# Kernel tuning notes

Measured on AMD Instinct MI355X. Metric: run time of the kernel, lower is better.

The kernel has to match this reference:

```python
import jax, jax.numpy as jnp
import numpy as np
import math

EPS = 1e-6          # eps for safe cumprod / clamping
CHUNK = 4           # chunk_size w
SHARP = 1.0         # sharpening_factor
NOISE_STD = 1.0
N_HEADS = 4
ADIM = 512


def moving_sum(x, back, forward):
    """Windowed running sum over last axis: out[k] = sum_{j=k-back}^{k+forward} x[j].
    Equivalent to the conv1d trick in the original (all-ones filter)."""
    k = x.shape[-1]
    pad = [(0, 0)] * (x.ndim - 1) + [(back, forward)]
    c = jnp.cumsum(jnp.pad(x, pad), axis=-1)
    c0 = jnp.concatenate([jnp.zeros_like(c[..., :1]), c], axis=-1)
    w = back + forward
    return c0[..., w + 1: w + 1 + k] - c0[..., :k]


def setup_inputs() -> dict:
    rng = jax.random.key(0)
    ks = jax.random.split(rng, 12)
    B, qlen, klen, kdim, qdim, adim = 8, 256, 2048, 512, 512, ADIM
    s = 0.02
    return {
        "key_enc": jax.random.normal(ks[0], (B, klen, kdim), jnp.float32),
        "query":   jax.random.normal(ks[1], (B, qlen, qdim), jnp.float32),
        "noise":   jax.random.normal(ks[2], (B, qlen, klen), jnp.float32),
        # monotonic energy params
        "Wk_m": jax.random.normal(ks[3], (kdim, adim), jnp.float32) * s,
        "bk_m": jnp.zeros((adim,), jnp.float32),
        "Wq_m": jax.random.normal(ks[4], (qdim, adim), jnp.float32) * s,
        "bq_m": jnp.zeros((adim,), jnp.float32),
        "r":    jnp.array([-4.0], jnp.float32),
        # chunkwise energy params (multi-head)
        "Wk_c": jax.random.normal(ks[5], (kdim, adim), jnp.float32) * s,
        "bk_c": jnp.zeros((adim,), jnp.float32),
        "Wq_c": jax.random.normal(ks[6], (qdim, adim), jnp.float32) * s,
        "bq_c": jnp.zeros((adim,), jnp.float32),
    }


def _mocha_beta(key_enc, query, noise, Wk_m, bk_m, Wq_m, bq_m, r,
                Wk_c, bk_c, Wq_c, bq_c):
    B, klen, _ = key_enc.shape
    qlen = query.shape[1]
    H = N_HEADS
    dk = ADIM // H
    scale = math.sqrt(ADIM)

    # --- monotonic energy (single head): [B, qlen, klen]
    k_m = key_enc @ Wk_m + bk_m
    q_m = query @ Wq_m + bq_m
    e_mono = jnp.einsum('bqa,bka->bqk', q_m, k_m) / scale + r[0]

    # --- p_choose with additive gaussian noise (encourages discreteness)
    p_choose = jax.nn.sigmoid(e_mono + noise * NOISE_STD)  # [B,q,k]

    # --- safe cumprod of (1 - p) via exclusive cumsum in log space
    log1mp = jnp.log(jnp.clip(1.0 - p_choose, EPS, 1.0))
    cumprod_1mp = jnp.exp(jnp.cumsum(log1mp, axis=-1) - log1mp)  # exclusive

    # --- monotonic alpha recurrence over query steps (parallel-mode MoChA)
    aw0 = jnp.zeros((B, klen), jnp.float32).at[:, 0].set(1.0)

    def step(aw_prev, inp):
        p_i, cp_i = inp  # [B, klen]
        alpha_i = p_i * cp_i * jnp.cumsum(
            aw_prev / jnp.clip(cp_i, EPS, 1.0), axis=-1)
        return alpha_i, alpha_i

    xs = (jnp.swapaxes(p_choose, 0, 1), jnp.swapaxes(cumprod_1mp, 0, 1))
    _, alpha_q = jax.lax.scan(step, aw0, xs)          # [q, B, k]
    alpha = jnp.swapaxes(alpha_q, 0, 1)                # [B, q, k]

    # --- chunkwise energy (multi-head): [B, H, q, k]
    k_c = (key_enc @ Wk_c + bk_c).reshape(B, klen, H, dk)
    q_c = (query @ Wq_c + bq_c).reshape(B, qlen, H, dk)
    e_chunk = jnp.einsum('bqhd,bkhd->bhqk', q_c, k_c) / scale

    # --- efficient chunkwise attention (clipped-logit moving-sum softmax)
    e = e_chunk - jnp.max(e_chunk, axis=3, keepdims=True)
    softmax_exp = jnp.maximum(jnp.exp(e), 1e-5)
    denom = moving_sum(softmax_exp, back=CHUNK - 1, forward=0)
    beta = softmax_exp * moving_sum(
        alpha[:, None] * SHARP / denom, back=0, forward=CHUNK - 1)
    return beta  # [B, H, q, k]


def reference(key_enc, query, noise, Wk_m, bk_m, Wq_m, bq_m, r,
              Wk_c, bk_c, Wq_c, bq_c):
    return _mocha_beta(key_enc, query, noise, Wk_m, bk_m, Wq_m, bq_m, r,
                       Wk_c, bk_c, Wq_c, bq_c)
```

## Files before the change

### kernel.cpp

```cpp
#include <hip/hip_runtime.h>
#include <math.h>

#define BATCH   8
#define QLEN    256
#define KLEN    2048
#define KDIM    512
#define NHEADS  4
#define DKH     128
#define NG      5
#define QROWS   (BATCH * QLEN)
#define GCOLS   (NG * 512)

static constexpr float INV_SCALE = 0.04419417382415922f;
static constexpr float EPSV = 1e-6f;

typedef __attribute__((ext_vector_type(8))) short bf16x8;
typedef __attribute__((ext_vector_type(4))) float f32x4;

__device__ __forceinline__ unsigned short f2bf(float f) {
    unsigned u = __builtin_bit_cast(unsigned, f);
    u += 0x7fffu + ((u >> 16) & 1u);
    return (unsigned short)(u >> 16);
}
__device__ __forceinline__ float bf2f(unsigned short u) {
    unsigned x = (unsigned)u << 16;
    return __builtin_bit_cast(float, x);
}

__device__ __forceinline__ void lds_barrier() {
    __asm__ volatile("s_waitcnt lgkmcnt(0)\n\ts_barrier" ::: "memory");
}

__device__ __forceinline__ void gload_lds16(const void* g, void* l) {
    __builtin_amdgcn_global_load_lds(
        (const __attribute__((address_space(1))) void*)g,
        (__attribute__((address_space(3))) void*)l, 16, 0, 0);
}

#define NKXB 8192
#define NQXB 1024
__global__ __launch_bounds__(256) void prep(
    const float* __restrict__ key_enc, const float* __restrict__ query,
    const float* __restrict__ Wk_m, const float* __restrict__ Wk_c,
    const float* __restrict__ Wq_m, const float* __restrict__ Wq_c,
    unsigned short* __restrict__ kx, unsigned short* __restrict__ qx,
    unsigned short* __restrict__ kwm, unsigned short* __restrict__ kwc,
    unsigned short* __restrict__ qwm, unsigned short* __restrict__ qwc)
{
    const int gb = blockIdx.x, tid = threadIdx.x;
    const float* x; unsigned short* y; int i;
    if (gb < NKXB)              { x = key_enc; y = kx; i = gb * 256 + tid; }
    else if (gb < NKXB + NQXB)  { x = query;   y = qx; i = (gb - NKXB) * 256 + tid; }
    else {
        const int w = gb - NKXB - NQXB;
        const int which = w >> 8;
        i = (w & 255) * 256 + tid;
        x = (which == 0) ? Wk_m : (which == 1) ? Wk_c : (which == 2) ? Wq_m : Wq_c;
        y = (which == 0) ? kwm  : (which == 1) ? kwc  : (which == 2) ? qwm  : qwc;
    }
    float4 v = ((const float4*)x)[i];
    ushort4 o;
    o.x = f2bf(v.x); o.y = f2bf(v.y); o.z = f2bf(v.z); o.w = f2bf(v.w);
    ((ushort4*)y)[i] = o;
}

__device__ __forceinline__ void mfma_nt_staged(
    const unsigned short* __restrict__ A, const unsigned short* __restrict__ B,
    int lda, int ldb, int bm, int bn,
    unsigned short* AsLDS, unsigned short* BsLDS, f32x4 acc[4][4], int ksteps)
{
    const int t = threadIdx.x;
    const int wv = t >> 6, ln = t & 63;
    const int r = ln & 15, quad = ln >> 4;
    const int wm = (wv >> 1) * 64, wn = (wv & 1) * 64;
    const int srow = wv * 16 + (ln >> 2);
    const int scol = (ln & 3) * 8;

    for (int ks = 0; ks < ksteps; ++ks) {
        const int k0 = ks * 32;
        #pragma unroll
        for (int j = 0; j < 2; ++j) {
            gload_lds16(A + (size_t)(bm + j * 64 + srow) * lda + k0 + scol,
                        AsLDS + (size_t)(j * 64 + wv * 16) * 32);
            gload_lds16(B + (size_t)(bn + j * 64 + srow) * ldb + k0 + scol,
                        BsLDS + (size_t)(j * 64 + wv * 16) * 32);
        }
        __syncthreads();
        bf16x8 af[4], bg[4];
        #pragma unroll
        for (int f = 0; f < 4; ++f)
            af[f] = *(const bf16x8*)(AsLDS + (size_t)(wm + f * 16 + r) * 32 + quad * 8);
        #pragma unroll
        for (int f = 0; f < 4; ++f)
            bg[f] = *(const bf16x8*)(BsLDS + (size_t)(wn + f * 16 + r) * 32 + quad * 8);
        #pragma unroll
        for (int i = 0; i < 4; ++i)
            #pragma unroll
            for (int j2 = 0; j2 < 4; ++j2)
                acc[i][j2] = __builtin_amdgcn_mfma_f32_16x16x32_bf16(
                    af[i], bg[j2], acc[i][j2], 0, 0, 0);
        __syncthreads();
    }
}

__device__ __forceinline__ void zero_acc(f32x4 acc[4][4]) {
    #pragma unroll
    for (int i = 0; i < 4; ++i)
        #pragma unroll
        for (int j = 0; j < 4; ++j)
            acc[i][j] = f32x4{0.f, 0.f, 0.f, 0.f};
}

__global__ __launch_bounds__(256) void smallg(
    const unsigned short* __restrict__ kwm, const unsigned short* __restrict__ kwc,
    const unsigned short* __restrict__ qwm, const unsigned short* __restrict__ qwc,
    const float* __restrict__ Wk_mf, const float* __restrict__ Wk_cf,
    const float* __restrict__ Wq_mf,
    const float* __restrict__ bq_m, const float* __restrict__ bk_m,
    const float* __restrict__ bq_c,
    unsigned short* __restrict__ GT, float* __restrict__ aux)
{
    __shared__ unsigned short As[128 * 32];
    __shared__ unsigned short Bs[128 * 32];
    __shared__ float red[256];
    const int blk = blockIdx.x, tid = threadIdx.x;

    if (blk < 80) {
        const int seg = blk >> 4, t = blk & 15;
        const int bm = (t >> 2) * 128, bn = (t & 3) * 128;
        const unsigned short *A, *B; int ks;
        if (seg == 0) { A = kwm; B = qwm; ks = 16; }
        else { const int h = seg - 1; A = kwc + h * 128; B = qwc + h * 128; ks = 4; }
        f32x4 acc[4][4]; zero_acc(acc);
        mfma_nt_staged(A, B, 512, 512, bm, bn, As, Bs, acc, ks);
        const int wv = tid >> 6, ln = tid & 63;
        const int r = ln & 15, quad = ln >> 4;
        const int m0 = bm + (wv >> 1) * 64, n0 = bn + (wv & 1) * 64;
        #pragma unroll
        for (int j = 0; j < 4; ++j) {
            const int n = n0 + j * 16 + r;
            #pragma unroll
            for (int i = 0; i < 4; ++i)
                #pragma unroll
                for (int reg = 0; reg < 4; ++reg) {
                    const int m = m0 + i * 16 + quad * 4 + reg;
                    GT[(size_t)(seg * 512 + m) * 512 + n] = f2bf(acc[i][j][reg]);
                }
        }
        return;
    }
    const int ab = blk - 80;
    if (ab < 2) {
        const int d = ab * 256 + tid;
        const float* row = Wk_mf + (size_t)d * 512;
        float s = 0.f;
        for (int j = 0; j < 512; j += 4) {
            float4 a = *(const float4*)(row + j);
            float4 b = *(const float4*)(bq_m + j);
            s += a.x * b.x + a.y * b.y + a.z * b.z + a.w * b.w;
        }
        aux[d] = s; return;
    }
    if (ab < 10) {
        const int t = ab - 2, h = t >> 1;
        const int d = (t & 1) * 256 + tid;
        const float* row = Wk_cf + (size_t)d * 512 + h * 128;
        const float* bv = bq_c + h * 128;
        float s = 0.f;
        for (int j = 0; j < 128; j += 4) {
            float4 a = *(const float4*)(row + j);
            float4 b = *(const float4*)(bv + j);
            s += a.x * b.x + a.y * b.y + a.z * b.z + a.w * b.w;
        }
        aux[512 + h * 512 + d] = s; return;
    }
    if (ab < 12) {
        const int d = (ab - 10) * 256 + tid;
        const float* row = Wq_mf + (size_t)d * 512;
        float s = 0.f;
        for (int j = 0; j < 512; j += 4) {
            float4 a = *(const float4*)(row + j);
            float4 b = *(const float4*)(bk_m + j);
            s += a.x * b.x + a.y * b.y + a.z * b.z + a.w * b.w;
        }
        aux[GCOLS + d] = s; return;
    }
    float s = bq_m[tid] * bk_m[tid] + bq_m[tid + 256] * bk_m[tid + 256];
    red[tid] = s; __syncthreads();
    for (int o = 128; o > 0; o >>= 1) {
        if (tid < o) red[tid] += red[tid + o];
        __syncthreads();
    }
    if (tid == 0) aux[GCOLS + 512] = red[0];
}

__global__ __launch_bounds__(256) void qg_kernel(
    const unsigned short* __restrict__ qx, const unsigned short* __restrict__ GT,
    const float* __restrict__ aux,
    unsigned short* __restrict__ qg, float* __restrict__ vq2)
{
    __shared__ unsigned short As[128 * 32];
    __shared__ unsigned short Bs[128 * 32];
    __shared__ float wuS[512];
    const int v = blockIdx.x, tid = threadIdx.x;
    if (v < 320) {
        const int by = v / 20, bx = v % 20;
        const int bm = by * 128, bn = bx * 128;
        f32x4 acc[4][4]; zero_acc(acc);
        mfma_nt_staged(qx, GT, 512, 512, bm, bn, As, Bs, acc, 16);
        const int wv = tid >> 6, ln = tid & 63;
        const int r = ln & 15, quad = ln >> 4;
        const int m0 = bm + (wv >> 1) * 64, n0 = bn + (wv & 1) * 64;
        #pragma unroll
        for (int j = 0; j < 4; ++j) {
            const int n = n0 + j * 16 + r;
            const float wvb = aux[n];
            #pragma unroll
            for (int i = 0; i < 4; ++i)
                #pragma unroll
                for (int reg = 0; reg < 4; ++reg) {
                    const int m = m0 + i * 16 + quad * 4 + reg;
                    qg[(size_t)m * GCOLS + n] = f2bf(acc[i][j][reg] + wvb);
                }
        }
        return;
    }
    wuS[tid] = aux[GCOLS + tid];
    wuS[tid + 256] = aux[GCOLS + tid + 256];
    __syncthreads();
    const float cc = aux[GCOLS + 512];
    const int q = (v - 320) * 256 + tid;
    const unsigned short* row = qx + (size_t)q * 512;
    float s = 0.f;
    for (int j = 0; j < 512; j += 4) {
        ushort4 a = *(const ushort4*)(row + j);
        s = fmaf(bf2f(a.x), wuS[j], s);
        s = fmaf(bf2f(a.y), wuS[j + 1], s);
        s = fmaf(bf2f(a.z), wuS[j + 2], s);
        s = fmaf(bf2f(a.w), wuS[j + 3], s);
    }
    vq2[q] = (s + cc) * INV_SCALE;
}

__global__ __launch_bounds__(256) void pchoose_mfma(
    const unsigned short* __restrict__ qg, const unsigned short* __restrict__ kx,
    const float* __restrict__ noise, const float* __restrict__ rp,
    const float* __restrict__ vq2, float* __restrict__ p)
{
    __shared__ unsigned short As[128 * 32];
    __shared__ unsigned short Bs[128 * 32];
    const int b = blockIdx.z;
    const unsigned short* A = qg + (size_t)b * QLEN * GCOLS;
    const unsigned short* B = kx + (size_t)b * KLEN * 512;
    const int bm = blockIdx.y * 128, bn = blockIdx.x * 128;
    f32x4 acc[4][4]; zero_acc(acc);
    mfma_nt_staged(A, B, GCOLS, 512, bm, bn, As, Bs, acc, 16);
    const int wv = threadIdx.x >> 6, ln = threadIdx.x & 63;
    const int r = ln & 15, quad = ln >> 4;
    const int m0 = bm + (wv >> 1) * 64, n0 = bn + (wv & 1) * 64;
    const float rv = rp[0];
    #pragma unroll
    for (int i = 0; i < 4; ++i) {
        #pragma unroll
        for (int reg = 0; reg < 4; ++reg) {
            const int q = m0 + i * 16 + quad * 4 + reg;
            const size_t rowoff = ((size_t)b * QLEN + q) * KLEN;
            const float vq = vq2[b * QLEN + q] + rv;
            #pragma unroll
            for (int j = 0; j < 4; ++j) {
                const int k = n0 + j * 16 + r;
                const float e = acc[i][j][reg] * INV_SCALE + vq + noise[rowoff + k];
                p[rowoff + k] = __builtin_amdgcn_rcpf(1.0f + __expf(-e));
            }
        }
    }
}

__device__ __forceinline__ float wave_incl_scan(float x)
{
#define DPP_ADD(ctrl, rmask, bctrl)                                            \
    { int _t = __builtin_amdgcn_update_dpp(0, __builtin_bit_cast(int, x),      \
                                           ctrl, rmask, 0xf, bctrl);           \
      x += __builtin_bit_cast(float, _t); }
    DPP_ADD(0x111, 0xf, true)
    DPP_ADD(0x112, 0xf, true)
    DPP_ADD(0x114, 0xf, true)
    DPP_ADD(0x118, 0xf, true)
    DPP_ADD(0x142, 0xa, false)
    DPP_ADD(0x143, 0xc, false)
#undef DPP_ADD
    return x;
}

__global__ __launch_bounds__(256) void cumprod_mr(
    const float* __restrict__ p, float* __restrict__ mArr, float* __restrict__ rArr)
{
    const size_t row = blockIdx.x;
    const float* pr = p + row * KLEN;
    float* mr = mArr + row * KLEN;
    float* rr = rArr + row * KLEN;
    const int tid = threadIdx.x;
    const int lane = tid & 63, wid = tid >> 6;
    __shared__ float waveTot[4];

    float4 v0 = *(const float4*)(pr + tid * 8);
    float4 v1 = *(const float4*)(pr + tid * 8 + 4);
    float pv[8] = {v0.x, v0.y, v0.z, v0.w, v1.x, v1.y, v1.z, v1.w};
    float excl[8];
    float run = 0.0f;
    #pragma unroll
    for (int j = 0; j < 8; ++j) {
        float l = __logf(fminf(fmaxf(1.0f - pv[j], EPSV), 1.0f));
        excl[j] = run;
        run += l;
    }
    float s = wave_incl_scan(run);
    if (lane == 63) waveTot[wid] = s;
    __syncthreads();
    float wex = 0.0f;
    for (int w = 0; w < wid; ++w) wex += waveTot[w];
    const float texcl = wex + s - run;

    float mv[8], rv[8];
    #pragma unroll
    for (int j = 0; j < 8; ++j) {
        const float cpv = __expf(texcl + excl[j]);
        mv[j] = pv[j] * cpv;
        rv[j] = __builtin_amdgcn_rcpf(fminf(fmaxf(cpv, EPSV), 1.0f));
    }
    *(float4*)(mr + tid * 8)     = *(float4*)&mv[0];
    *(float4*)(mr + tid * 8 + 4) = *(float4*)&mv[4];
    *(float4*)(rr + tid * 8)     = *(float4*)&rv[0];
    *(float4*)(rr + tid * 8 + 4) = *(float4*)&rv[4];
}

__global__ __launch_bounds__(512, 1) void alpha_echunk(
    const float* __restrict__ mArr, const float* __restrict__ rArr,
    float* __restrict__ alpha,
    const unsigned short* __restrict__ qg, const unsigned short* __restrict__ kx,
    float* __restrict__ out)
{
    __shared__ __align__(16) char smem[98304];
    const int bid = blockIdx.x;
    const int tid = threadIdx.x;

    if (bid < BATCH) {
        __builtin_amdgcn_s_setprio(1);
        float (*wt)[8] = (float (*)[8])smem;
        const int lane = tid & 63, wid = tid >> 6;
        const float* mrow = mArr + (size_t)bid * QLEN * KLEN + tid * 4;
        const float* rrow = rArr + (size_t)bid * QLEN * KLEN + tid * 4;
        float* arow = alpha + (size_t)bid * QLEN * KLEN + tid * 4;

        float aw0 = 0.f, aw1 = 0.f, aw2 = 0.f, aw3 = 0.f;
        if (tid == 0) aw0 = 1.0f;

        float4 mA = *(const float4*)(mrow);
        float4 rA = *(const float4*)(rrow);
        float4 mB = *(const float4*)(mrow + KLEN);
        float4 rB = *(const float4*)(rrow + KLEN);

#define ASTEP(I, MREG, RREG)                                                   \
    {                                                                          \
        const int i_ = (I);                                                    \
        float4 mc = MREG, rc = RREG;                                           \
        const int rn_ = (i_ + 2 < QLEN) ? (i_ + 2) : (QLEN - 1);               \
        MREG = *(const float4*)(mrow + (size_t)rn_ * KLEN);                    \
        RREG = *(const float4*)(rrow + (size_t)rn_ * KLEN);                    \
        float run = 0.0f, i0, i1, i2, i3;                                      \
        run = fmaf(aw0, rc.x, run); i0 = run;                                  \
        run = fmaf(aw1, rc.y, run); i1 = run;                                  \
        run = fmaf(aw2, rc.z, run); i2 = run;                                  \
        run = fmaf(aw3, rc.w, run); i3 = run;                                  \
        float tot = wave_incl_scan(run);                                       \
        if (lane == 63) wt[i_ & 1][wid] = tot;                                 \
        lds_barrier();                                                         \
        float base = tot - run;                                                \
        float4 w0 = *(const float4*)&wt[i_ & 1][0];                            \
        float4 w1 = *(const float4*)&wt[i_ & 1][4];                            \
        if (wid > 0) base += w0.x;                                             \
        if (wid > 1) base += w0.y;                                             \
        if (wid > 2) base += w0.z;                                             \
        if (wid > 3) base += w0.w;                                             \
        if (wid > 4) base += w1.x;                                             \
        if (wid > 5) base += w1.y;                                             \
        if (wid > 6) base += w1.z;                                             \
        aw0 = mc.x * (base + i0);                                              \
        aw1 = mc.y * (base + i1);                                              \
        aw2 = mc.z * (base + i2);                                              \
        aw3 = mc.w * (base + i3);                                              \
        float4 ov; ov.x = aw0; ov.y = aw1; ov.z = aw2; ov.w = aw3;             \
        *(float4*)(arow + (size_t)i_ * KLEN) = ov;                             \
    }

        for (int io = 0; io < QLEN; io += 2) {
            ASTEP(io + 0, mA, rA)
            ASTEP(io + 1, mB, rB)
        }
#undef ASTEP
        __builtin_amdgcn_s_setprio(0);
        return;
    }

    const int v = bid - BATCH;
    const int z = v >> 4;
    const int rest = v & 15;
    const int by = rest >> 3;
    const int bx = rest & 7;
    const int b = z >> 2, h = z & 3;
    unsigned short* As = (unsigned short*)smem;
    unsigned short* Bs = (unsigned short*)(smem + 8192);
    const unsigned short* A = qg + (size_t)(b * QLEN) * GCOLS + 512 + h * 512;
    const unsigned short* B = kx + (size_t)b * KLEN * 512;
    const int bm = by * 128, bn = bx * 256;

    const int wv8 = tid >> 6, ln = tid & 63;
    const int r = ln & 15, quad = ln >> 4;
    const int wr = wv8 >> 2, wc = wv8 & 3;
    const int srow = tid >> 2;
    const int scol = (ln & 3) * 8;

    f32x4 acc[4][4]; zero_acc(acc);
    for (int ks = 0; ks < 16; ++ks) {
        const int k0 = ks * 32;
        gload_lds16(A + (size_t)(bm + srow) * GCOLS + k0 + scol,
                    As + (size_t)wv8 * 512);
        gload_lds16(B + (size_t)(bn + srow) * 512 + k0 + scol,
                    Bs + (size_t)wv8 * 512);
        gload_lds16(B + (size_t)(bn + 128 + srow) * 512 + k0 + scol,
                    Bs + 4096 + (size_t)wv8 * 512);
        __syncthreads();
        bf16x8 af[4], bg[4];
        #pragma unroll
        for (int f = 0; f < 4; ++f)
            af[f] = *(const bf16x8*)(As + (size_t)(wr * 64 + f * 16 + r) * 32 + quad * 8);
        #pragma unroll
        for (int f = 0; f < 4; ++f)
            bg[f] = *(const bf16x8*)(Bs + (size_t)(wc * 64 + f * 16 + r) * 32 + quad * 8);
        #pragma unroll
        for (int i = 0; i < 4; ++i)
            #pragma unroll
            for (int j2 = 0; j2 < 4; ++j2)
                acc[i][j2] = __builtin_amdgcn_mfma_f32_16x16x32_bf16(
                    af[i], bg[j2], acc[i][j2], 0, 0, 0);
        __syncthreads();
    }
    {
        const int m0 = bm + wr * 64, n0 = bn + wc * 64;
        #pragma unroll
        for (int i = 0; i < 4; ++i) {
            #pragma unroll
            for (int reg = 0; reg < 4; ++reg) {
                const int q = m0 + i * 16 + quad * 4 + reg;
                const size_t rowoff = ((size_t)z * QLEN + q) * KLEN;
                #pragma unroll
                for (int j = 0; j < 4; ++j) {
                    const int k = n0 + j * 16 + r;
                    out[rowoff + k] = acc[i][j][reg] * INV_SCALE;
                }
            }
        }
    }
}

__global__ __launch_bounds__(256) void beta_kernel(
    float* __restrict__ eo, const float* __restrict__ alpha)
{
    __shared__ float sse[KLEN + 3];
    __shared__ float su[KLEN + 3];
    __shared__ float wmax[4];

    const int tid = threadIdx.x;
    const int lane = tid & 63, wid = tid >> 6;
    const int row = blockIdx.x;
    const int q = row & (QLEN - 1);
    const int b = row >> 10;
    float* erow = eo + (size_t)row * KLEN;
    const float* arow = alpha + ((size_t)b * QLEN + q) * KLEN;

    if (tid < 3) { sse[tid] = 0.0f; su[KLEN + tid] = 0.0f; }

    float ev[8];
    float lm = -INFINITY;
    #pragma unroll
    for (int j = 0; j < 8; ++j) {
        const int k = tid + 256 * j;
        ev[j] = erow[k];
        lm = fmaxf(lm, ev[j]);
    }
    #pragma unroll
    for (int off = 32; off > 0; off >>= 1) lm = fmaxf(lm, __shfl_xor(lm, off));
    if (lane == 0) wmax[wid] = lm;
    __syncthreads();
    const float mx = fmaxf(fmaxf(wmax[0], wmax[1]), fmaxf(wmax[2], wmax[3]));

    #pragma unroll
    for (int j = 0; j < 8; ++j) {
        const int k = tid + 256 * j;
        sse[k + 3] = fmaxf(__expf(ev[j] - mx), 1e-5f);
    }
    __syncthreads();

    #pragma unroll
    for (int j = 0; j < 8; ++j) {
        const int k = tid + 256 * j;
        const float denom = sse[k + 3] + sse[k + 2] + sse[k + 1] + sse[k];
        su[k] = arow[k] * __builtin_amdgcn_rcpf(denom);
    }
    __syncthreads();

    #pragma unroll
    for (int j = 0; j < 8; ++j) {
        const int k = tid + 256 * j;
        erow[k] = sse[k + 3] * (su[k] + su[k + 1] + su[k + 2] + su[k + 3]);
    }
}

extern "C" void kernel_launch(void* const* d_in, const int* in_sizes, int n_in,
                              void* d_out, int out_size, void* d_ws, size_t ws_size,
                              hipStream_t stream)
{
    (void)in_sizes; (void)n_in; (void)out_size; (void)ws_size;
    const float* key_enc = (const float*)d_in[0];
    const float* query   = (const float*)d_in[1];
    const float* noise   = (const float*)d_in[2];
    const float* Wk_m    = (const float*)d_in[3];
    const float* bk_m    = (const float*)d_in[4];
    const float* Wq_m    = (const float*)d_in[5];
    const float* bq_m    = (const float*)d_in[6];
    const float* rp      = (const float*)d_in[7];
    const float* Wk_c    = (const float*)d_in[8];
    const float* bk_c    = (const float*)d_in[9];
    const float* Wq_c    = (const float*)d_in[10];
    const float* bq_c    = (const float*)d_in[11];
    float* out = (float*)d_out;
    (void)bk_c;

    char* w = (char*)d_ws;
    unsigned short* kx   = (unsigned short*)w; w += (size_t)BATCH * KLEN * KDIM * 2;
    unsigned short* qx   = (unsigned short*)w; w += (size_t)QROWS * KDIM * 2;
    unsigned short* kwm  = (unsigned short*)w; w += (size_t)512 * 512 * 2;
    unsigned short* kwc  = (unsigned short*)w; w += (size_t)512 * 512 * 2;
    unsigned short* qwm  = (unsigned short*)w; w += (size_t)512 * 512 * 2;
    unsigned short* qwc  = (unsigned short*)w; w += (size_t)512 * 512 * 2;
    unsigned short* GT   = (unsigned short*)w; w += (size_t)GCOLS * 512 * 2;
    unsigned short* qg   = (unsigned short*)w; w += (size_t)QROWS * GCOLS * 2;
    float* aux    = (float*)w; w += 4096 * 4;
    float* vq2    = (float*)w; w += QROWS * 4;
    float* p_alpha = (float*)w; w += (size_t)BATCH * QLEN * KLEN * 4;
    float* mArr    = (float*)w; w += (size_t)BATCH * QLEN * KLEN * 4;
    float* rArr    = (float*)w;

    hipLaunchKernelGGL(prep, dim3(NKXB + NQXB + 1024), dim3(256), 0, stream,
                       key_enc, query, Wk_m, Wk_c, Wq_m, Wq_c,
                       kx, qx, kwm, kwc, qwm, qwc);

    hipLaunchKernelGGL(smallg, dim3(93), dim3(256), 0, stream,
                       kwm, kwc, qwm, qwc, Wk_m, Wk_c, Wq_m,
                       bq_m, bk_m, bq_c, GT, aux);

    hipLaunchKernelGGL(qg_kernel, dim3(328), dim3(256), 0, stream,
                       qx, GT, aux, qg, vq2);

    hipLaunchKernelGGL(pchoose_mfma, dim3(KLEN / 128, QLEN / 128, BATCH), dim3(256), 0, stream,
                       qg, kx, noise, rp, vq2, p_alpha);

    hipLaunchKernelGGL(cumprod_mr, dim3(BATCH * QLEN), dim3(256), 0, stream,
                       p_alpha, mArr, rArr);

    hipLaunchKernelGGL(alpha_echunk, dim3(BATCH + 512), dim3(512), 0, stream,
                       mArr, rArr, p_alpha, qg, kx, out);

    hipLaunchKernelGGL(beta_kernel, dim3(BATCH * NHEADS * QLEN), dim3(256), 0, stream,
                       out, p_alpha);
}
```

Baseline: 282.9 us.

## Fuse two alpha recurrence steps per barrier via algebraic scan composition

Restructures the sequential alpha scan so each block barrier advances two query rows instead of one. The second row's prefix sum is expressed as an affine function of the first row's cross-wave offset, computed with three wave scans and a small 8-lane prefix over per-wave totals. This halves the number of workgroup barriers on the serial critical path. In exchange it adds more arithmetic and DPP scans per step, and regroups the floating-point sums slightly differently.

New measurement: 279.2 us. Within noise of the previous version (-1.3%).

```diff
diff --git a/kernel.cpp b/kernel.cpp
--- a/kernel.cpp
+++ b/kernel.cpp
@@ -292,6 +292,19 @@
     return x;
 }
 
+__device__ __forceinline__ float row_prefix8(float x)
+{
+#define DPP_ADD(ctrl)                                                          \
+    { int _t = __builtin_amdgcn_update_dpp(0, __builtin_bit_cast(int, x),      \
+                                           ctrl, 0xf, 0xf, true);              \
+      x += __builtin_bit_cast(float, _t); }
+    DPP_ADD(0x111)
+    DPP_ADD(0x112)
+    DPP_ADD(0x114)
+#undef DPP_ADD
+    return x;
+}
+
 __global__ __launch_bounds__(256) void cumprod_mr(
     const float* __restrict__ p, float* __restrict__ mArr, float* __restrict__ rArr)
 {
@@ -346,7 +359,7 @@
 
     if (bid < BATCH) {
         __builtin_amdgcn_s_setprio(1);
-        float (*wt)[8] = (float (*)[8])smem;
+        float* slots = (float*)smem;
         const int lane = tid & 63, wid = tid >> 6;
         const float* mrow = mArr + (size_t)bid * QLEN * KLEN + tid * 4;
         const float* rrow = rArr + (size_t)bid * QLEN * KLEN + tid * 4;
@@ -355,49 +368,83 @@
         float aw0 = 0.f, aw1 = 0.f, aw2 = 0.f, aw3 = 0.f;
         if (tid == 0) aw0 = 1.0f;
 
-        float4 mA = *(const float4*)(mrow);
-        float4 rA = *(const float4*)(rrow);
-        float4 mB = *(const float4*)(mrow + KLEN);
-        float4 rB = *(const float4*)(rrow + KLEN);
-
-#define ASTEP(I, MREG, RREG)                                                   \
+        float4 mP0 = *(const float4*)(mrow);
+        float4 rP0 = *(const float4*)(rrow);
+        float4 mP1 = *(const float4*)(mrow + KLEN);
+        float4 rP1 = *(const float4*)(rrow + KLEN);
+        float4 mQ0 = *(const float4*)(mrow + 2 * (size_t)KLEN);
+        float4 rQ0 = *(const float4*)(rrow + 2 * (size_t)KLEN);
+        float4 mQ1 = *(const float4*)(mrow + 3 * (size_t)KLEN);
+        float4 rQ1 = *(const float4*)(rrow + 3 * (size_t)KLEN);
+
+#define APAIR(I, M0, R0, M1, R1)                                               \
     {                                                                          \
-        const int i_ = (I);                                                    \
-        float4 mc = MREG, rc = RREG;                                           \
-        const int rn_ = (i_ + 2 < QLEN) ? (i_ + 2) : (QLEN - 1);               \
-        MREG = *(const float4*)(mrow + (size_t)rn_ * KLEN);                    \
-        RREG = *(const float4*)(rrow + (size_t)rn_ * KLEN);                    \
-        float run = 0.0f, i0, i1, i2, i3;                                      \
-        run = fmaf(aw0, rc.x, run); i0 = run;                                  \
-        run = fmaf(aw1, rc.y, run); i1 = run;                                  \
-        run = fmaf(aw2, rc.z, run); i2 = run;                                  \
-        run = fmaf(aw3, rc.w, run); i3 = run;                                  \
-        float tot = wave_incl_scan(run);                                       \
-        if (lane == 63) wt[i_ & 1][wid] = tot;                                 \
+        const int i_ = (I);                               \
+        float4 mc0 = M0, rc0 = R0, mc1 = M1, rc1 = R1;                         \
+        const int rn_ = (i_ + 4 < QLEN) ? (i_ + 4) : (QLEN - 2);               \
+        M0 = *(const float4*)(mrow + (size_t)rn_ * KLEN);                      \
+        R0 = *(const float4*)(rrow + (size_t)rn_ * KLEN);                      \
+        M1 = *(const float4*)(mrow + (size_t)(rn_ + 1) * KLEN);               \
+        R1 = *(const float4*)(rrow + (size_t)(rn_ + 1) * KLEN);               \
+                                 \
+        float run = 0.f, i0, i1, i2, i3;                                       \
+        run = fmaf(aw0, rc0.x, run); i0 = run;                                 \
+        run = fmaf(aw1, rc0.y, run); i1 = run;                                 \
+        run = fmaf(aw2, rc0.z, run); i2 = run;                                 \
+        run = fmaf(aw3, rc0.w, run); i3 = run;                                 \
+        const float sx = wave_incl_scan(run);                                  \
+        const float wb = sx - run;                                             \
+        const float W0 = wb + i0, W1 = wb + i1, W2 = wb + i2, W3 = wb + i3;    \
+                      \
+        const float u0 = mc0.x * rc1.x, u1 = mc0.y * rc1.y;                    \
+        const float u2 = mc0.z * rc1.z, u3 = mc0.w * rc1.w;                    \
+        float ur = u0;       const float U0 = ur;                              \
+        ur += u1;            const float U1 = ur;                              \
+        ur += u2;            const float U2 = ur;                              \
+        ur += u3;            const float U3 = ur;                              \
+        const float sU = wave_incl_scan(ur);                                   \
+        const float ub = sU - ur;                                              \
+        float vr = u0 * W0;              const float V0 = vr;                  \
+        vr = fmaf(u1, W1, vr);           const float V1 = vr;                  \
+        vr = fmaf(u2, W2, vr);           const float V2 = vr;                  \
+        vr = fmaf(u3, W3, vr);           const float V3 = vr;                  \
+        const float sV = wave_incl_scan(vr);                                   \
+        const float vb = sV - vr;                                              \
+        const int par = (i_ >> 1) & 1;                                         \
+        if (lane == 63) {                                                      \
+            float4 tv; tv.x = sx; tv.y = sU; tv.z = sV; tv.w = 0.f;            \
+            *(float4*)(slots + (par * 8 + wid) * 4) = tv;                      \
+        }                                                                      \
         lds_barrier();                                                         \
-        float base = tot - run;                                                \
-        float4 w0 = *(const float4*)&wt[i_ & 1][0];                            \
-        float4 w1 = *(const float4*)&wt[i_ & 1][4];                            \
-        if (wid > 0) base += w0.x;                                             \
-        if (wid > 1) base += w0.y;                                             \
-        if (wid > 2) base += w0.z;                                             \
-        if (wid > 3) base += w0.w;                                             \
-        if (wid > 4) base += w1.x;                                             \
-        if (wid > 5) base += w1.y;                                             \
-        if (wid > 6) base += w1.z;                                             \
-        aw0 = mc.x * (base + i0);                                              \
-        aw1 = mc.y * (base + i1);                                              \
-        aw2 = mc.z * (base + i2);                                              \
-        aw3 = mc.w * (base + i3);                                              \
-        float4 ov; ov.x = aw0; ov.y = aw1; ov.z = aw2; ov.w = aw3;             \
-        *(float4*)(arow + (size_t)i_ * KLEN) = ov;                             \
-    }
-
-        for (int io = 0; io < QLEN; io += 2) {
-            ASTEP(io + 0, mA, rA)
-            ASTEP(io + 1, mB, rB)
-        }
-#undef ASTEP
+        float4 tr = *(const float4*)(slots + (par * 8 + (lane & 7)) * 4);      \
+        const float pT = row_prefix8(tr.x);                                    \
+        const float Cex = pT - tr.x;                                           \
+        const float t2 = fmaf(Cex, tr.y, tr.z);                                \
+        const float pQ = row_prefix8(t2);                                      \
+        const float C2ex = pQ - t2;                                            \
+        const float b0 = __shfl(Cex, wid);                                     \
+        const float b1 = __shfl(C2ex, wid);                                    \
+                                                          \
+        float4 o0;                                                             \
+        o0.x = mc0.x * (b0 + W0); o0.y = mc0.y * (b0 + W1);                    \
+        o0.z = mc0.z * (b0 + W2); o0.w = mc0.w * (b0 + W3);                    \
+        *(float4*)(arow + (size_t)i_ * KLEN) = o0;                             \
+                                                        \
+        const float X0 = fmaf(b0, ub + U0, vb + V0);                           \
+        const float X1 = fmaf(b0, ub + U1, vb + V1);                           \
+        const float X2 = fmaf(b0, ub + U2, vb + V2);                           \
+        const float X3 = fmaf(b0, ub + U3, vb + V3);                           \
+        aw0 = mc1.x * (b1 + X0); aw1 = mc1.y * (b1 + X1);                      \
+        aw2 = mc1.z * (b1 + X2); aw3 = mc1.w * (b1 + X3);                      \
+        float4 o1; o1.x = aw0; o1.y = aw1; o1.z = aw2; o1.w = aw3;             \
+        *(float4*)(arow + (size_t)(i_ + 1) * KLEN) = o1;                       \
+    }
+
+        for (int io = 0; io < QLEN; io += 4) {
+            APAIR(io + 0, mP0, rP0, mP1, rP1)
+            APAIR(io + 2, mQ0, rQ0, mQ1, rQ1)
+        }
+#undef APAIR
         __builtin_amdgcn_s_setprio(0);
         return;
     }
```
